# Performance work log

Measured on AMD Instinct MI355X. Metric: run time of the kernel, lower is better.

The kernel has to match this reference:

```python
import jax, jax.numpy as jnp
import numpy as np

NUM_HEADS = 16
EMB = 1024
HEAD_DIM = EMB // NUM_HEADS


def setup_inputs() -> dict:
    key = jax.random.key(0)
    ks = jax.random.split(key, 9)
    N, L = 2, 2048
    return {
        "keys": jax.random.normal(ks[0], (N, L, EMB), dtype=jnp.float32),
        "queries": jax.random.normal(ks[1], (N, L, EMB), dtype=jnp.float32),
        "values": jax.random.normal(ks[2], (N, L, EMB), dtype=jnp.float32),
        "mask": jax.random.randint(ks[3], (N, L), 0, 2, dtype=jnp.int32),
        "Wk": jax.random.normal(ks[4], (HEAD_DIM, HEAD_DIM), dtype=jnp.float32) * 0.05,
        "Wq": jax.random.normal(ks[5], (HEAD_DIM, HEAD_DIM), dtype=jnp.float32) * 0.05,
        "Wv": jax.random.normal(ks[6], (HEAD_DIM, HEAD_DIM), dtype=jnp.float32) * 0.05,
        "Wo": jax.random.normal(ks[7], (EMB, EMB), dtype=jnp.float32) * 0.02,
        "bo": jax.random.normal(ks[8], (EMB,), dtype=jnp.float32) * 0.02,
    }


def reference(keys, queries, values, mask, Wk, Wq, Wv, Wo, bo):
    N, Q, E = queries.shape
    H, D = NUM_HEADS, HEAD_DIM
    # reshape to heads: [N, L, H, D]
    k = keys.reshape(N, -1, H, D) @ Wk.T
    q = queries.reshape(N, -1, H, D) @ Wq.T
    # faithful to source bug: values are the v-projection of the projected queries
    v = q @ Wv.T
    # energy: [N, H, Q, K]
    energy = jnp.einsum("nqhd,nkhd->nhqk", q, k)
    m = mask[:, None, None, :]  # [N,1,1,K]
    energy = jnp.where(m == 0, jnp.float32(-1e20), energy)
    p = jax.nn.softmax(energy / jnp.sqrt(jnp.float32(E)), axis=3)
    attn = jnp.einsum("nhqk,nkhd->nqhd", p, v).reshape(N, Q, E)
    return attn @ Wo.T + bo
```

## Files before the change

kernel.cpp:

```cpp
#include <hip/hip_runtime.h>
#include <hip/hip_bf16.h>
#include <cmath>

constexpr int N_ = 2;
constexpr int L_ = 2048;
constexpr int H_ = 16;
constexpr int E_ = 1024;
constexpr int ROWS_ = N_ * L_ * H_;
constexpr float KSCALE = 0.04508422002778010648f;

typedef __attribute__((ext_vector_type(8))) short bf16x8;
typedef __attribute__((ext_vector_type(4))) float f32x4;
typedef unsigned short ushort_t;
#define MFMA16(a, b, c) __builtin_amdgcn_mfma_f32_16x16x32_bf16(a, b, c, 0, 0, 0)

__device__ __forceinline__ unsigned short f2bf(float x) {
    union { float f; unsigned u; } v; v.f = x;
    return (unsigned short)((v.u + 0x7fffu + ((v.u >> 16) & 1u)) >> 16);
}
__device__ __forceinline__ unsigned pack2(float a, float b) {
    __hip_bfloat162 t = __float22bfloat162_rn(make_float2(a, b));
    union { __hip_bfloat162 h; unsigned u; } v; v.h = t;
    return v.u;
}

__global__ __launch_bounds__(256) void proj_kernel(
    const float* __restrict__ keys, const float* __restrict__ queries,
    const float* __restrict__ Wk, const float* __restrict__ Wq, const float* __restrict__ Wv,
    ushort_t* __restrict__ qo, ushort_t* __restrict__ ko, ushort_t* __restrict__ vto)
{
    constexpr int P = 72;
    __shared__ __align__(16) ushort_t Xq[64 * P];
    __shared__ __align__(16) ushort_t Xk[64 * P];
    __shared__ __align__(16) ushort_t Wqs[64 * P];
    __shared__ __align__(16) ushort_t Wks[64 * P];
    __shared__ __align__(16) ushort_t Wvs[64 * P];
    const int tid = threadIdx.x;
    const int lt = blockIdx.x & 31;
    const int h  = (blockIdx.x >> 5) & 15;
    const int n  = blockIdx.x >> 9;
    const int r0 = tid >> 4, c4 = (tid & 15) * 4;

#pragma unroll
    for (int j = 0; j < 4; ++j) {
        const int r = r0 + 16 * j;
        const size_t xoff = (size_t)(n * L_ + lt * 64 + r) * E_ + h * 64 + c4;
        const float4 xq = *(const float4*)&queries[xoff];
        const float4 xk = *(const float4*)&keys[xoff];
        const float4 wq = *(const float4*)&Wq[r * 64 + c4];
        const float4 wk = *(const float4*)&Wk[r * 64 + c4];
        const float4 wv = *(const float4*)&Wv[r * 64 + c4];
        *(uint2*)&Xq[r * P + c4]  = make_uint2(pack2(xq.x, xq.y), pack2(xq.z, xq.w));
        *(uint2*)&Xk[r * P + c4]  = make_uint2(pack2(xk.x, xk.y), pack2(xk.z, xk.w));
        *(uint2*)&Wqs[r * P + c4] = make_uint2(pack2(wq.x, wq.y), pack2(wq.z, wq.w));
        *(uint2*)&Wks[r * P + c4] = make_uint2(pack2(wk.x, wk.y), pack2(wk.z, wk.w));
        *(uint2*)&Wvs[r * P + c4] = make_uint2(pack2(wv.x, wv.y), pack2(wv.z, wv.w));
    }
    __syncthreads();

    const int wave = tid >> 6, lane = tid & 63;
    const int quad = lane >> 4, l16 = lane & 15;
    const int arow = (wave * 16 + l16) * P;
    const f32x4 zero = (f32x4){0.f, 0.f, 0.f, 0.f};

    bf16x8 a0 = *(const bf16x8*)&Xq[arow + quad * 8];
    bf16x8 a1 = *(const bf16x8*)&Xq[arow + 32 + quad * 8];
    bf16x8 c0 = *(const bf16x8*)&Xk[arow + quad * 8];
    bf16x8 c1 = *(const bf16x8*)&Xk[arow + 32 + quad * 8];
    f32x4 qf[4], kf[4];
#pragma unroll
    for (int nt = 0; nt < 4; ++nt) {
        const int brow = (nt * 16 + l16) * P;
        f32x4 acc = MFMA16(a0, *(const bf16x8*)&Wqs[brow + quad * 8], zero);
        qf[nt] = MFMA16(a1, *(const bf16x8*)&Wqs[brow + 32 + quad * 8], acc);
        acc = MFMA16(c0, *(const bf16x8*)&Wks[brow + quad * 8], zero);
        kf[nt] = MFMA16(c1, *(const bf16x8*)&Wks[brow + 32 + quad * 8], acc);
    }
    __syncthreads();

    const int crow = wave * 16 + quad * 4;
#pragma unroll
    for (int nt = 0; nt < 4; ++nt)
#pragma unroll
        for (int reg = 0; reg < 4; ++reg) {
            Xq[(crow + reg) * P + nt * 16 + l16]  = f2bf(qf[nt][reg]);
            Wqs[(crow + reg) * P + nt * 16 + l16] = f2bf(kf[nt][reg] * KSCALE);
        }
    asm volatile("s_waitcnt lgkmcnt(0)" ::: "memory");

    bf16x8 va0 = *(const bf16x8*)&Xq[arow + quad * 8];
    bf16x8 va1 = *(const bf16x8*)&Xq[arow + 32 + quad * 8];
    f32x4 vf[4];
#pragma unroll
    for (int nt = 0; nt < 4; ++nt) {
        const int brow = (nt * 16 + l16) * P;
        f32x4 acc = MFMA16(va0, *(const bf16x8*)&Wvs[brow + quad * 8], zero);
        vf[nt] = MFMA16(va1, *(const bf16x8*)&Wvs[brow + 32 + quad * 8], acc);
    }
#pragma unroll
    for (int nt = 0; nt < 4; ++nt)
#pragma unroll
        for (int reg = 0; reg < 4; ++reg)
            Xk[(nt * 16 + l16) * P + crow + reg] = f2bf(vf[nt][reg]);
    __syncthreads();

#pragma unroll
    for (int j = 0; j < 4; ++j) {
        const int r = r0 + 16 * j;
        const size_t qkoff = (size_t)(n * L_ + lt * 64 + r) * E_ + h * 64 + c4;
        *(uint2*)&qo[qkoff] = *(const uint2*)&Xq[r * P + c4];
        *(uint2*)&ko[qkoff] = *(const uint2*)&Wqs[r * P + c4];
        const size_t vtoff = ((size_t)(n * H_ + h) * 64 + r) * L_ + lt * 64 + c4;
        *(uint2*)&vto[vtoff] = *(const uint2*)&Xk[r * P + c4];
    }
}

__global__ __launch_bounds__(256) void attn_kernel(
    const ushort_t* __restrict__ q, const ushort_t* __restrict__ k,
    const ushort_t* __restrict__ vt, const float* __restrict__ maskf,
    ushort_t* __restrict__ attn)
{
    constexpr int P = 72;
    __shared__ __align__(16) ushort_t Ks[2][64 * P];
    __shared__ __align__(16) ushort_t VTs[2][64 * P];
    __shared__ __align__(16) ushort_t Ps[128 * P];
    __shared__ float Ls[128];

    const int g = blockIdx.x;
    const int xcd = g & 7, j0 = g >> 3;
    const int nh = xcd * 4 + (j0 & 3);
    const int qt = j0 >> 2;
    const int n = nh >> 4, h = nh & 15;

    const int tid = threadIdx.x;
    const int wave = tid >> 6, lane = tid & 63;
    const int l16 = lane & 15, quad = lane >> 4;
    const int r0 = tid >> 4, c4 = (tid & 15) * 4;

    const ushort_t* kh = k  + (size_t)n * L_ * E_ + h * 64;
    const ushort_t* vh = vt + (size_t)(n * H_ + h) * 64 * L_;
    const float*    mh = maskf + n * L_;
    const size_t qrow0 = (size_t)n * L_ + qt * 128 + wave * 32;

    bf16x8 qb[2][2];
#pragma unroll
    for (int s = 0; s < 2; ++s)
#pragma unroll
        for (int c = 0; c < 2; ++c)
            qb[s][c] = *(const bf16x8*)&q[(qrow0 + s * 16 + l16) * E_ + h * 64 + c * 32 + quad * 8];

    uint2 kr[4], vr[4];
#pragma unroll
    for (int j = 0; j < 4; ++j) {
        const int r = r0 + 16 * j;
        kr[j] = *(const uint2*)&kh[(size_t)r * E_ + c4];
        vr[j] = *(const uint2*)&vh[(size_t)r * L_ + c4];
    }
    f32x4 mf[4];
#pragma unroll
    for (int mk = 0; mk < 4; ++mk) mf[mk] = *(const f32x4*)&mh[mk * 16 + quad * 4];

#pragma unroll
    for (int j = 0; j < 4; ++j) {
        const int r = r0 + 16 * j;
        *(uint2*)&Ks[0][r * P + c4]  = kr[j];
        *(uint2*)&VTs[0][r * P + c4] = vr[j];
    }
    __syncthreads();

    float lacc[2] = {0.f, 0.f};
    f32x4 O[2][4];
#pragma unroll
    for (int s = 0; s < 2; ++s)
#pragma unroll
        for (int dt = 0; dt < 4; ++dt) O[s][dt] = (f32x4){0.f, 0.f, 0.f, 0.f};

    for (int t = 0; t < 32; ++t) {
        const int cur = t & 1, nxt = cur ^ 1;
        const int tn = (t < 31) ? t + 1 : 31;

#pragma unroll
        for (int j = 0; j < 4; ++j) {
            const int r = r0 + 16 * j;
            kr[j] = *(const uint2*)&kh[(size_t)(tn * 64 + r) * E_ + c4];
            vr[j] = *(const uint2*)&vh[(size_t)r * L_ + tn * 64 + c4];
        }
        f32x4 mfn[4];
#pragma unroll
        for (int mk = 0; mk < 4; ++mk)
            mfn[mk] = *(const f32x4*)&mh[tn * 64 + mk * 16 + quad * 4];

        bf16x8 kA[4][2];
#pragma unroll
        for (int mk = 0; mk < 4; ++mk)
#pragma unroll
            for (int c = 0; c < 2; ++c)
                kA[mk][c] = *(const bf16x8*)&Ks[cur][(mk * 16 + l16) * P + c * 32 + quad * 8];

        f32x4 sA[2][4];
#pragma unroll
        for (int s = 0; s < 2; ++s)
#pragma unroll
            for (int mk = 0; mk < 4; ++mk) {
                f32x4 acc = mf[mk];
                acc = MFMA16(kA[mk][0], qb[s][0], acc);
                sA[s][mk] = MFMA16(kA[mk][1], qb[s][1], acc);
            }

#pragma unroll
        for (int s = 0; s < 2; ++s)
#pragma unroll
            for (int mk = 0; mk < 4; ++mk) {
                const float p0 = __builtin_amdgcn_exp2f(sA[s][mk][0]);
                const float p1 = __builtin_amdgcn_exp2f(sA[s][mk][1]);
                const float p2 = __builtin_amdgcn_exp2f(sA[s][mk][2]);
                const float p3 = __builtin_amdgcn_exp2f(sA[s][mk][3]);
                lacc[s] += (p0 + p1) + (p2 + p3);
                *(uint2*)&Ps[(wave * 32 + s * 16 + l16) * P + mk * 16 + quad * 4] =
                    make_uint2(pack2(p0, p1), pack2(p2, p3));
            }
        asm volatile("s_waitcnt lgkmcnt(0)" ::: "memory");

        bf16x8 vB[4][2];
#pragma unroll
        for (int dt = 0; dt < 4; ++dt)
#pragma unroll
            for (int c = 0; c < 2; ++c)
                vB[dt][c] = *(const bf16x8*)&VTs[cur][(dt * 16 + l16) * P + c * 32 + quad * 8];
        bf16x8 pa[2][2];
#pragma unroll
        for (int s = 0; s < 2; ++s)
#pragma unroll
            for (int c = 0; c < 2; ++c)
                pa[s][c] = *(const bf16x8*)&Ps[(wave * 32 + s * 16 + l16) * P + c * 32 + quad * 8];
#pragma unroll
        for (int s = 0; s < 2; ++s)
#pragma unroll
            for (int dt = 0; dt < 4; ++dt) {
                O[s][dt] = MFMA16(pa[s][0], vB[dt][0], O[s][dt]);
                O[s][dt] = MFMA16(pa[s][1], vB[dt][1], O[s][dt]);
            }

#pragma unroll
        for (int j = 0; j < 4; ++j) {
            const int r = r0 + 16 * j;
            *(uint2*)&Ks[nxt][r * P + c4]  = kr[j];
            *(uint2*)&VTs[nxt][r * P + c4] = vr[j];
        }
#pragma unroll
        for (int mk = 0; mk < 4; ++mk) mf[mk] = mfn[mk];
        __syncthreads();
    }

#pragma unroll
    for (int s = 0; s < 2; ++s) {
        float v = lacc[s];
        v += __shfl_xor(v, 16);
        v += __shfl_xor(v, 32);
        if (quad == 0) Ls[wave * 32 + s * 16 + l16] = 1.f / v;
    }
    asm volatile("s_waitcnt lgkmcnt(0)" ::: "memory");
    f32x4 linv[2];
#pragma unroll
    for (int s = 0; s < 2; ++s) linv[s] = *(const f32x4*)&Ls[wave * 32 + s * 16 + quad * 4];

#pragma unroll
    for (int s = 0; s < 2; ++s)
#pragma unroll
        for (int dt = 0; dt < 4; ++dt)
#pragma unroll
            for (int reg = 0; reg < 4; ++reg) {
                const size_t row = qrow0 + s * 16 + quad * 4 + reg;
                attn[row * E_ + h * 64 + dt * 16 + l16] = f2bf(O[s][dt][reg] * linv[s][reg]);
            }
}

__global__ __launch_bounds__(256) void conv_misc_kernel(
    const float* __restrict__ Wo, const int* __restrict__ mask,
    ushort_t* __restrict__ Wob, float* __restrict__ maskf)
{
    if (blockIdx.x < 1024) {
        const int i = (blockIdx.x * 256 + threadIdx.x) * 4;
        const float4 w = *(const float4*)&Wo[i];
        *(uint2*)&Wob[i] = make_uint2(pack2(w.x, w.y), pack2(w.z, w.w));
    } else {
        const int j = (blockIdx.x - 1024) * 256 + threadIdx.x;
        if (j < N_ * L_) maskf[j] = mask[j] ? 0.f : -1e9f;
    }
}

__global__ __launch_bounds__(256) void outproj_kernel(
    const ushort_t* __restrict__ attn, const ushort_t* __restrict__ Wob,
    const float* __restrict__ bo, float* __restrict__ out)
{
    constexpr int P = 72;
    __shared__ __align__(16) ushort_t As[128 * P];
    __shared__ __align__(16) ushort_t Bs[64 * P];
    const int tid = threadIdx.x;
    const int bc = (blockIdx.x & 15) * 64;
    const int br = (blockIdx.x >> 4) * 128;
    const int r0 = tid >> 4, c4 = (tid & 15) * 4;
    const int wave = tid >> 6, lane = tid & 63;
    const int quad = lane >> 4, l16 = lane & 15;

    uint2 ar[8], brg[4];
#pragma unroll
    for (int j = 0; j < 8; ++j)
        ar[j] = *(const uint2*)&attn[(size_t)(br + r0 + 16 * j) * E_ + c4];
#pragma unroll
    for (int j = 0; j < 4; ++j)
        brg[j] = *(const uint2*)&Wob[(size_t)(bc + r0 + 16 * j) * E_ + c4];

    f32x4 acc[2][4];
#pragma unroll
    for (int s = 0; s < 2; ++s)
#pragma unroll
        for (int nt = 0; nt < 4; ++nt) acc[s][nt] = (f32x4){0.f, 0.f, 0.f, 0.f};

    for (int kt = 0; kt < 16; ++kt) {
#pragma unroll
        for (int j = 0; j < 8; ++j) *(uint2*)&As[(r0 + 16 * j) * P + c4] = ar[j];
#pragma unroll
        for (int j = 0; j < 4; ++j) *(uint2*)&Bs[(r0 + 16 * j) * P + c4] = brg[j];
        __syncthreads();
        const int knext = ((kt < 15) ? (kt + 1) : kt) * 64;
#pragma unroll
        for (int j = 0; j < 8; ++j)
            ar[j] = *(const uint2*)&attn[(size_t)(br + r0 + 16 * j) * E_ + knext + c4];
#pragma unroll
        for (int j = 0; j < 4; ++j)
            brg[j] = *(const uint2*)&Wob[(size_t)(bc + r0 + 16 * j) * E_ + knext + c4];

        bf16x8 aw[2][2], bw[4][2];
#pragma unroll
        for (int s = 0; s < 2; ++s)
#pragma unroll
            for (int c = 0; c < 2; ++c)
                aw[s][c] = *(const bf16x8*)&As[(wave * 32 + s * 16 + l16) * P + c * 32 + quad * 8];
#pragma unroll
        for (int nt = 0; nt < 4; ++nt)
#pragma unroll
            for (int c = 0; c < 2; ++c)
                bw[nt][c] = *(const bf16x8*)&Bs[(nt * 16 + l16) * P + c * 32 + quad * 8];
#pragma unroll
        for (int s = 0; s < 2; ++s)
#pragma unroll
            for (int nt = 0; nt < 4; ++nt) {
                acc[s][nt] = MFMA16(aw[s][0], bw[nt][0], acc[s][nt]);
                acc[s][nt] = MFMA16(aw[s][1], bw[nt][1], acc[s][nt]);
            }
        __syncthreads();
    }
#pragma unroll
    for (int s = 0; s < 2; ++s)
#pragma unroll
        for (int nt = 0; nt < 4; ++nt) {
            const float bias = bo[bc + nt * 16 + l16];
#pragma unroll
            for (int reg = 0; reg < 4; ++reg)
                out[(size_t)(br + wave * 32 + s * 16 + quad * 4 + reg) * E_ + bc + nt * 16 + l16] =
                    acc[s][nt][reg] + bias;
        }
}

extern "C" void kernel_launch(void* const* d_in, const int* in_sizes, int n_in,
                              void* d_out, int out_size, void* d_ws, size_t ws_size,
                              hipStream_t stream)
{
    const float* keys    = (const float*)d_in[0];
    const float* queries = (const float*)d_in[1];
    const int*   mask    = (const int*)d_in[3];
    const float* Wk      = (const float*)d_in[4];
    const float* Wq      = (const float*)d_in[5];
    const float* Wv      = (const float*)d_in[6];
    const float* Wo      = (const float*)d_in[7];
    const float* bo      = (const float*)d_in[8];
    float* out = (float*)d_out;

    ushort_t* qbf  = (ushort_t*)d_ws;
    ushort_t* kbf  = qbf + (size_t)ROWS_ * 64;
    ushort_t* vtbf = kbf + (size_t)ROWS_ * 64;
    ushort_t* abf  = vtbf + (size_t)ROWS_ * 64;
    ushort_t* wob  = abf + (size_t)ROWS_ * 64;
    float*    mskf = (float*)(wob + (size_t)E_ * E_);

    conv_misc_kernel<<<1024 + (N_ * L_ + 255) / 256, 256, 0, stream>>>(Wo, mask, wob, mskf);
    proj_kernel<<<N_ * H_ * (L_ / 64), 256, 0, stream>>>(keys, queries, Wk, Wq, Wv,
                                                         qbf, kbf, vtbf);
    attn_kernel<<<N_ * H_ * (L_ / 128), 256, 0, stream>>>(qbf, kbf, vtbf, mskf, abf);
    outproj_kernel<<<(N_ * L_ / 128) * (E_ / 64), 256, 0, stream>>>(abf, wob, bo, out);
}
```

Measured before the change: 196.5 us.

## Split attention over key halves with separate combine kernel and single-buffered LDS

Splits the attention key loop into two halves handled by separate blocks, doubling the grid, and writes unnormalised fp16 partial outputs plus row sums that a new combine kernel adds and normalises into bf16. LDS K/V is reduced from double to single buffering and occupancy is requested at 4 blocks per SU. The mask and Wo bf16 conversion kernels are removed: the mask is converted inline in attention and Wo is converted while loading in outproj. This aims at better occupancy and fewer launches, at the cost of extra global traffic for partials, an added combine launch, and one more barrier per iteration.

Measured after the change: 259.4 us. 1.32x slower.

```diff
diff --git a/kernel.cpp b/kernel.cpp
--- a/kernel.cpp
+++ b/kernel.cpp
@@ -1,5 +1,6 @@
 #include <hip/hip_runtime.h>
 #include <hip/hip_bf16.h>
+#include <hip/hip_fp16.h>
 #include <cmath>
 
 constexpr int N_ = 2;
@@ -21,6 +22,11 @@
 __device__ __forceinline__ unsigned pack2(float a, float b) {
     __hip_bfloat162 t = __float22bfloat162_rn(make_float2(a, b));
     union { __hip_bfloat162 h; unsigned u; } v; v.h = t;
+    return v.u;
+}
+__device__ __forceinline__ ushort_t f2h(float x) {
+    __half h = __float2half(x);
+    union { __half h; ushort_t u; } v; v.h = h;
     return v.u;
 }
 
@@ -115,22 +121,28 @@
     }
 }
 
-__global__ __launch_bounds__(256) void attn_kernel(
+__global__ __launch_bounds__(256, 4) void attn_kernel(
     const ushort_t* __restrict__ q, const ushort_t* __restrict__ k,
-    const ushort_t* __restrict__ vt, const float* __restrict__ maskf,
-    ushort_t* __restrict__ attn)
+    const ushort_t* __restrict__ vt, const int* __restrict__ mask,
+    ushort_t* __restrict__ Oa, ushort_t* __restrict__ Ob,
+    float* __restrict__ la, float* __restrict__ lb)
 {
     constexpr int P = 72;
-    __shared__ __align__(16) ushort_t Ks[2][64 * P];
-    __shared__ __align__(16) ushort_t VTs[2][64 * P];
+    __shared__ __align__(16) ushort_t Ks[64 * P];
+    __shared__ __align__(16) ushort_t VTs[64 * P];
     __shared__ __align__(16) ushort_t Ps[128 * P];
-    __shared__ float Ls[128];
 
     const int g = blockIdx.x;
     const int xcd = g & 7, j0 = g >> 3;
     const int nh = xcd * 4 + (j0 & 3);
-    const int qt = j0 >> 2;
+    const int rest = j0 >> 2;
+    const int qt = rest & 15;
+    const int half = rest >> 4;
     const int n = nh >> 4, h = nh & 15;
+    const int t0 = half * 16;
+
+    ushort_t* __restrict__ Op = half ? Ob : Oa;
+    float*    __restrict__ lp = half ? lb : la;
 
     const int tid = threadIdx.x;
     const int wave = tid >> 6, lane = tid & 63;
@@ -139,7 +151,7 @@
 
     const ushort_t* kh = k  + (size_t)n * L_ * E_ + h * 64;
     const ushort_t* vh = vt + (size_t)(n * H_ + h) * 64 * L_;
-    const float*    mh = maskf + n * L_;
+    const int*      mh = mask + n * L_;
     const size_t qrow0 = (size_t)n * L_ + qt * 128 + wave * 32;
 
     bf16x8 qb[2][2];
@@ -153,20 +165,16 @@
 #pragma unroll
     for (int j = 0; j < 4; ++j) {
         const int r = r0 + 16 * j;
-        kr[j] = *(const uint2*)&kh[(size_t)r * E_ + c4];
-        vr[j] = *(const uint2*)&vh[(size_t)r * L_ + c4];
+        kr[j] = *(const uint2*)&kh[(size_t)(t0 * 64 + r) * E_ + c4];
+        vr[j] = *(const uint2*)&vh[(size_t)r * L_ + t0 * 64 + c4];
     }
     f32x4 mf[4];
 #pragma unroll
-    for (int mk = 0; mk < 4; ++mk) mf[mk] = *(const f32x4*)&mh[mk * 16 + quad * 4];
-
-#pragma unroll
-    for (int j = 0; j < 4; ++j) {
-        const int r = r0 + 16 * j;
-        *(uint2*)&Ks[0][r * P + c4]  = kr[j];
-        *(uint2*)&VTs[0][r * P + c4] = vr[j];
-    }
-    __syncthreads();
+    for (int mk = 0; mk < 4; ++mk) {
+        const int4 mi = *(const int4*)&mh[t0 * 64 + mk * 16 + quad * 4];
+        mf[mk] = (f32x4){mi.x ? 0.f : -1e9f, mi.y ? 0.f : -1e9f,
+                         mi.z ? 0.f : -1e9f, mi.w ? 0.f : -1e9f};
+    }
 
     float lacc[2] = {0.f, 0.f};
     f32x4 O[2][4];
@@ -175,10 +183,16 @@
 #pragma unroll
         for (int dt = 0; dt < 4; ++dt) O[s][dt] = (f32x4){0.f, 0.f, 0.f, 0.f};
 
-    for (int t = 0; t < 32; ++t) {
-        const int cur = t & 1, nxt = cur ^ 1;
-        const int tn = (t < 31) ? t + 1 : 31;
-
+    for (int t = t0; t < t0 + 16; ++t) {
+#pragma unroll
+        for (int j = 0; j < 4; ++j) {
+            const int r = r0 + 16 * j;
+            *(uint2*)&Ks[r * P + c4]  = kr[j];
+            *(uint2*)&VTs[r * P + c4] = vr[j];
+        }
+        __syncthreads();
+
+        const int tn = (t < t0 + 15) ? t + 1 : t;
 #pragma unroll
         for (int j = 0; j < 4; ++j) {
             const int r = r0 + 16 * j;
@@ -187,15 +201,18 @@
         }
         f32x4 mfn[4];
 #pragma unroll
+        for (int mk = 0; mk < 4; ++mk) {
+            const int4 mi = *(const int4*)&mh[tn * 64 + mk * 16 + quad * 4];
+            mfn[mk] = (f32x4){mi.x ? 0.f : -1e9f, mi.y ? 0.f : -1e9f,
+                              mi.z ? 0.f : -1e9f, mi.w ? 0.f : -1e9f};
+        }
+
+        bf16x8 kA[4][2];
+#pragma unroll
         for (int mk = 0; mk < 4; ++mk)
-            mfn[mk] = *(const f32x4*)&mh[tn * 64 + mk * 16 + quad * 4];
-
-        bf16x8 kA[4][2];
-#pragma unroll
-        for (int mk = 0; mk < 4; ++mk)
 #pragma unroll
             for (int c = 0; c < 2; ++c)
-                kA[mk][c] = *(const bf16x8*)&Ks[cur][(mk * 16 + l16) * P + c * 32 + quad * 8];
+                kA[mk][c] = *(const bf16x8*)&Ks[(mk * 16 + l16) * P + c * 32 + quad * 8];
 
         f32x4 sA[2][4];
 #pragma unroll
@@ -226,7 +243,7 @@
         for (int dt = 0; dt < 4; ++dt)
 #pragma unroll
             for (int c = 0; c < 2; ++c)
-                vB[dt][c] = *(const bf16x8*)&VTs[cur][(dt * 16 + l16) * P + c * 32 + quad * 8];
+                vB[dt][c] = *(const bf16x8*)&VTs[(dt * 16 + l16) * P + c * 32 + quad * 8];
         bf16x8 pa[2][2];
 #pragma unroll
         for (int s = 0; s < 2; ++s)
@@ -240,13 +257,6 @@
                 O[s][dt] = MFMA16(pa[s][0], vB[dt][0], O[s][dt]);
                 O[s][dt] = MFMA16(pa[s][1], vB[dt][1], O[s][dt]);
             }
-
-#pragma unroll
-        for (int j = 0; j < 4; ++j) {
-            const int r = r0 + 16 * j;
-            *(uint2*)&Ks[nxt][r * P + c4]  = kr[j];
-            *(uint2*)&VTs[nxt][r * P + c4] = vr[j];
-        }
 #pragma unroll
         for (int mk = 0; mk < 4; ++mk) mf[mk] = mfn[mk];
         __syncthreads();
@@ -257,13 +267,9 @@
         float v = lacc[s];
         v += __shfl_xor(v, 16);
         v += __shfl_xor(v, 32);
-        if (quad == 0) Ls[wave * 32 + s * 16 + l16] = 1.f / v;
-    }
-    asm volatile("s_waitcnt lgkmcnt(0)" ::: "memory");
-    f32x4 linv[2];
-#pragma unroll
-    for (int s = 0; s < 2; ++s) linv[s] = *(const f32x4*)&Ls[wave * 32 + s * 16 + quad * 4];
-
+        if (quad == 0)
+            lp[((size_t)(n * H_ + h)) * L_ + qt * 128 + wave * 32 + s * 16 + l16] = v;
+    }
 #pragma unroll
     for (int s = 0; s < 2; ++s)
 #pragma unroll
@@ -271,26 +277,33 @@
 #pragma unroll
             for (int reg = 0; reg < 4; ++reg) {
                 const size_t row = qrow0 + s * 16 + quad * 4 + reg;
-                attn[row * E_ + h * 64 + dt * 16 + l16] = f2bf(O[s][dt][reg] * linv[s][reg]);
+                Op[row * E_ + h * 64 + dt * 16 + l16] = f2h(O[s][dt][reg]);
             }
 }
 
-__global__ __launch_bounds__(256) void conv_misc_kernel(
-    const float* __restrict__ Wo, const int* __restrict__ mask,
-    ushort_t* __restrict__ Wob, float* __restrict__ maskf)
+__global__ __launch_bounds__(256) void combine_kernel(
+    const ushort_t* __restrict__ Oa, const ushort_t* __restrict__ Ob,
+    const float* __restrict__ la, const float* __restrict__ lb,
+    ushort_t* __restrict__ abf)
 {
-    if (blockIdx.x < 1024) {
-        const int i = (blockIdx.x * 256 + threadIdx.x) * 4;
-        const float4 w = *(const float4*)&Wo[i];
-        *(uint2*)&Wob[i] = make_uint2(pack2(w.x, w.y), pack2(w.z, w.w));
-    } else {
-        const int j = (blockIdx.x - 1024) * 256 + threadIdx.x;
-        if (j < N_ * L_) maskf[j] = mask[j] ? 0.f : -1e9f;
-    }
+    const size_t i = ((size_t)blockIdx.x * 256 + threadIdx.x) * 4;
+    const int row = (int)(i >> 10);
+    const int col = (int)(i & 1023);
+    const int h = col >> 6;
+    const int n = row >> 11, l = row & 2047;
+    const size_t lidx = ((size_t)(n * H_ + h)) * L_ + l;
+    const float inv = 1.f / (la[lidx] + lb[lidx]);
+    const __half2* A2 = (const __half2*)&Oa[i];
+    const __half2* B2 = (const __half2*)&Ob[i];
+    const float2 a0 = __half22float2(A2[0]), a1 = __half22float2(A2[1]);
+    const float2 b0 = __half22float2(B2[0]), b1 = __half22float2(B2[1]);
+    *(uint2*)&abf[i] = make_uint2(
+        pack2((a0.x + b0.x) * inv, (a0.y + b0.y) * inv),
+        pack2((a1.x + b1.x) * inv, (a1.y + b1.y) * inv));
 }
 
 __global__ __launch_bounds__(256) void outproj_kernel(
-    const ushort_t* __restrict__ attn, const ushort_t* __restrict__ Wob,
+    const ushort_t* __restrict__ attn, const float* __restrict__ Wo,
     const float* __restrict__ bo, float* __restrict__ out)
 {
     constexpr int P = 72;
@@ -303,13 +316,13 @@
     const int wave = tid >> 6, lane = tid & 63;
     const int quad = lane >> 4, l16 = lane & 15;
 
-    uint2 ar[8], brg[4];
+    uint2 ar[8]; float4 wr[4];
 #pragma unroll
     for (int j = 0; j < 8; ++j)
         ar[j] = *(const uint2*)&attn[(size_t)(br + r0 + 16 * j) * E_ + c4];
 #pragma unroll
     for (int j = 0; j < 4; ++j)
-        brg[j] = *(const uint2*)&Wob[(size_t)(bc + r0 + 16 * j) * E_ + c4];
+        wr[j] = *(const float4*)&Wo[(size_t)(bc + r0 + 16 * j) * E_ + c4];
 
     f32x4 acc[2][4];
 #pragma unroll
@@ -321,7 +334,9 @@
 #pragma unroll
         for (int j = 0; j < 8; ++j) *(uint2*)&As[(r0 + 16 * j) * P + c4] = ar[j];
 #pragma unroll
-        for (int j = 0; j < 4; ++j) *(uint2*)&Bs[(r0 + 16 * j) * P + c4] = brg[j];
+        for (int j = 0; j < 4; ++j)
+            *(uint2*)&Bs[(r0 + 16 * j) * P + c4] =
+                make_uint2(pack2(wr[j].x, wr[j].y), pack2(wr[j].z, wr[j].w));
         __syncthreads();
         const int knext = ((kt < 15) ? (kt + 1) : kt) * 64;
 #pragma unroll
@@ -329,7 +344,7 @@
             ar[j] = *(const uint2*)&attn[(size_t)(br + r0 + 16 * j) * E_ + knext + c4];
 #pragma unroll
         for (int j = 0; j < 4; ++j)
-            brg[j] = *(const uint2*)&Wob[(size_t)(bc + r0 + 16 * j) * E_ + knext + c4];
+            wr[j] = *(const float4*)&Wo[(size_t)(bc + r0 + 16 * j) * E_ + knext + c4];
 
         bf16x8 aw[2][2], bw[4][2];
 #pragma unroll
@@ -378,15 +393,18 @@
     float* out = (float*)d_out;
 
     ushort_t* qbf  = (ushort_t*)d_ws;
-    ushort_t* kbf  = qbf + (size_t)ROWS_ * 64;
-    ushort_t* vtbf = kbf + (size_t)ROWS_ * 64;
-    ushort_t* abf  = vtbf + (size_t)ROWS_ * 64;
-    ushort_t* wob  = abf + (size_t)ROWS_ * 64;
-    float*    mskf = (float*)(wob + (size_t)E_ * E_);
-
-    conv_misc_kernel<<<1024 + (N_ * L_ + 255) / 256, 256, 0, stream>>>(Wo, mask, wob, mskf);
+    ushort_t* kbf  = qbf  + (size_t)ROWS_ * 64;
+    ushort_t* vtbf = kbf  + (size_t)ROWS_ * 64;
+    ushort_t* Oa   = vtbf + (size_t)ROWS_ * 64;
+    ushort_t* Ob   = Oa   + (size_t)ROWS_ * 64;
+    ushort_t* abf  = Ob   + (size_t)ROWS_ * 64;
+    float*    la   = (float*)(abf + (size_t)ROWS_ * 64);
+    float*    lb   = la + (size_t)N_ * H_ * L_;
+
     proj_kernel<<<N_ * H_ * (L_ / 64), 256, 0, stream>>>(keys, queries, Wk, Wq, Wv,
                                                          qbf, kbf, vtbf);
-    attn_kernel<<<N_ * H_ * (L_ / 128), 256, 0, stream>>>(qbf, kbf, vtbf, mskf, abf);
-    outproj_kernel<<<(N_ * L_ / 128) * (E_ / 64), 256, 0, stream>>>(abf, wob, bo, out);
-}
+    attn_kernel<<<N_ * H_ * (L_ / 128) * 2, 256, 0, stream>>>(qbf, kbf, vtbf, mask,
+                                                              Oa, Ob, la, lb);
+    combine_kernel<<<(N_ * L_ * E_ / 4) / 256, 256, 0, stream>>>(Oa, Ob, la, lb, abf);
+    outproj_kernel<<<(N_ * L_ / 128) * (E_ / 64), 256, 0, stream>>>(abf, Wo, bo, out);
+}
```
